# Performance work log

Hardware: AMD Instinct MI355X
Metric: run time of the kernel (lower is better)

Reference implementation:

```python
import jax, jax.numpy as jnp
import numpy as np

B = 32768   # batch
T = 10      # n_track
NW = 3      # n_waypoints
D = 128     # d_model
H = 8       # num_heads
HD = D // H # head_dim = 16


def _ln(x, g, b, eps=1e-5):
    m = jnp.mean(x, axis=-1, keepdims=True)
    v = jnp.mean((x - m) ** 2, axis=-1, keepdims=True)
    return (x - m) * jax.lax.rsqrt(v + eps) * g + b


def setup_inputs() -> dict:
    key = jax.random.key(0)
    ks = jax.random.split(key, 16)
    rn = lambda k, shape, s=0.05: jax.random.normal(k, shape, dtype=jnp.float32) * s
    return {
        "track_left": jax.random.normal(ks[0], (B, T, 2), dtype=jnp.float32),
        "track_right": jax.random.normal(ks[1], (B, T, 2), dtype=jnp.float32),
        "coord_w": rn(ks[2], (D, 2), 0.5), "coord_b": jnp.zeros((D,), jnp.float32),
        "pos_emb": rn(ks[3], (T, D), 0.02),
        "side_emb": rn(ks[4], (2, D), 0.02),
        "query_emb": rn(ks[5], (NW, D), 0.02),
        "tokens_ln_g": jnp.ones((D,), jnp.float32), "tokens_ln_b": jnp.zeros((D,), jnp.float32),
        "queries_ln_g": jnp.ones((D,), jnp.float32), "queries_ln_b": jnp.zeros((D,), jnp.float32),
        "in_proj_w": rn(ks[6], (3 * D, D)), "in_proj_b": jnp.zeros((3 * D,), jnp.float32),
        "out_proj_w": rn(ks[7], (D, D)), "out_proj_b": jnp.zeros((D,), jnp.float32),
        "fc1_w": rn(ks[8], (2 * D, D)), "fc1_b": jnp.zeros((2 * D,), jnp.float32),
        "fc2_w": rn(ks[9], (D, 2 * D)), "fc2_b": jnp.zeros((D,), jnp.float32),
        "post_attn_ln_g": jnp.ones((D,), jnp.float32), "post_attn_ln_b": jnp.zeros((D,), jnp.float32),
        "post_ffn_ln_g": jnp.ones((D,), jnp.float32), "post_ffn_ln_b": jnp.zeros((D,), jnp.float32),
        "head_w": rn(ks[10], (2, D)), "head_b": jnp.zeros((2,), jnp.float32),
    }


def reference(track_left, track_right, coord_w, coord_b, pos_emb, side_emb,
              query_emb, tokens_ln_g, tokens_ln_b, queries_ln_g, queries_ln_b,
              in_proj_w, in_proj_b, out_proj_w, out_proj_b, fc1_w, fc1_b,
              fc2_w, fc2_b, post_attn_ln_g, post_attn_ln_b, post_ffn_ln_g,
              post_ffn_ln_b, head_w, head_b):
    # --- tokens: embed + add pos/side + LN ---  (dropout = eval-mode identity)
    coords = jnp.concatenate([track_left, track_right], axis=1)       # [B, 2T, 2]
    coord_feat = coords @ coord_w.T + coord_b                          # [B, 2T, D]
    pos_vecs = jnp.concatenate([pos_emb, pos_emb], axis=0)             # [2T, D]
    side_vecs = jnp.concatenate([
        jnp.broadcast_to(side_emb[0], (T, D)),
        jnp.broadcast_to(side_emb[1], (T, D))], axis=0)                # [2T, D]
    tokens = _ln(coord_feat + pos_vecs + side_vecs, tokens_ln_g, tokens_ln_b)  # [B, 2T, D]

    # --- queries (shared across batch) ---
    queries = _ln(query_emb, queries_ln_g, queries_ln_b)               # [NW, D]

    # --- MHA (batch_first, packed qkv in_proj as in nn.MultiheadAttention) ---
    wq, wk, wv = in_proj_w[:D], in_proj_w[D:2 * D], in_proj_w[2 * D:]
    bq, bk, bv = in_proj_b[:D], in_proj_b[D:2 * D], in_proj_b[2 * D:]
    q = (queries @ wq.T + bq).reshape(NW, H, HD)                       # [NW, H, HD]
    k = (tokens @ wk.T + bk).reshape(-1, 2 * T, H, HD)                 # [B, 2T, H, HD]
    v = (tokens @ wv.T + bv).reshape(-1, 2 * T, H, HD)                 # [B, 2T, H, HD]
    scores = jnp.einsum('whd,bkhd->bhwk', q, k) / jnp.sqrt(jnp.float32(HD))
    attn = jax.nn.softmax(scores, axis=-1)                             # [B, H, NW, 2T]
    ctx = jnp.einsum('bhwk,bkhd->bwhd', attn, v).reshape(-1, NW, D)    # [B, NW, D]
    attn_out = ctx @ out_proj_w.T + out_proj_b                         # [B, NW, D]

    # --- residual + LN + FFN + residual + LN + head ---
    x = _ln(queries[None, :, :] + attn_out, post_attn_ln_g, post_attn_ln_b)
    h = jax.nn.relu(x @ fc1_w.T + fc1_b)
    h = h @ fc2_w.T + fc2_b
    x = _ln(x + h, post_ffn_ln_g, post_ffn_ln_b)
    return x @ head_w.T + head_b                                       # [B, NW, 2]
```

## Files before the change

kernel.cpp:

```cpp
#include <hip/hip_runtime.h>
#include <hip/hip_bf16.h>


typedef __bf16 bf16x8 __attribute__((ext_vector_type(8)));
typedef float  f32x4  __attribute__((ext_vector_type(4)));
static_assert(sizeof(bf16x8) == 16, "bf16x8 must be 16B");

__device__ __forceinline__ unsigned short f2b(float x) {
  __bf16 h = (__bf16)x;
  return __builtin_bit_cast(unsigned short, h);
}
__device__ __forceinline__ float b2f(unsigned short u) {
  return (float)__builtin_bit_cast(__bf16, u);
}
__device__ __forceinline__ float dot4(float4 a, float4 b) {
  return a.x*b.x + a.y*b.y + a.z*b.z + a.w*b.w;
}
__device__ __forceinline__ f32x4 mfma16(bf16x8 a, bf16x8 b, f32x4 c) {
  return __builtin_amdgcn_mfma_f32_16x16x32_bf16(a, b, c, 0, 0, 0);
}

#define WS_OM    0
#define WS_FC1   49152
#define WS_FC2   114688
#define WS_VB    180224
#define WS_VU    190464
#define WS_VW    190976
#define WS_VC    191488
#define WS_QN    192000
#define WS_SB    193536
#define WS_SU    195456
#define WS_SCAL  195744
#define WS_SUB   195756
#define WS_SWB   195836
#define WS_SBB   195916

__device__ float mean128(float v, volatile float* red) {
  #pragma unroll
  for (int o = 32; o; o >>= 1) v += __shfl_down(v, o, 64);
  __syncthreads();
  if ((threadIdx.x & 63) == 0) red[threadIdx.x >> 6] = v;
  __syncthreads();
  return (red[0] + red[1]) * (1.0f / 128.0f);
}

__global__ void k_tables(
    const float* __restrict__ coord_w, const float* __restrict__ coord_b,
    const float* __restrict__ pos_emb, const float* __restrict__ side_emb,
    const float* __restrict__ query_emb,
    const float* __restrict__ tln_g, const float* __restrict__ tln_b,
    const float* __restrict__ qln_g, const float* __restrict__ qln_b,
    const float* __restrict__ ipw, const float* __restrict__ ipb,
    char* __restrict__ ws)
{
  __shared__ float red[2];
  __shared__ float qn[3][128];
  __shared__ float qmat[3][128];
  __shared__ float vecA[128];
  __shared__ float vecB[128];
  __shared__ float vecC[128];
  __shared__ float kuA[128];
  __shared__ float kwA[128];
  __shared__ float kcA[128];
  const int d = threadIdx.x;
  const int t = blockIdx.x;

  float u  = coord_w[d*2+0];
  float w2 = coord_w[d*2+1];
  float g  = tln_g[d];
  float mu = mean128(u,  red);
  float mw = mean128(w2, red);
  float uh = u - mu, wh = w2 - mw;

  #pragma unroll
  for (int w = 0; w < 3; w++) {
    float qe = query_emb[w*128 + d];
    float m  = mean128(qe, red);
    float m2 = mean128(qe*qe, red);
    float var = m2 - m*m;
    qn[w][d] = (qe - m) * rsqrtf(var + 1e-5f) * qln_g[d] + qln_b[d];
  }
  __syncthreads();
  {
    const float* wqr = ipw + d*128;
    float a0 = 0, a1 = 0, a2 = 0;
    for (int k4 = 0; k4 < 32; k4++) {
      float4 wv4 = *(const float4*)&wqr[k4*4];
      a0 += dot4(wv4, *(const float4*)&qn[0][k4*4]);
      a1 += dot4(wv4, *(const float4*)&qn[1][k4*4]);
      a2 += dot4(wv4, *(const float4*)&qn[2][k4*4]);
    }
    float bq = ipb[d];
    qmat[0][d] = a0 + bq; qmat[1][d] = a1 + bq; qmat[2][d] = a2 + bq;
  }
  __syncthreads();

  if (t < 20) {
    float base = coord_b[d] + pos_emb[(t % 10)*128 + d] + side_emb[(t < 10 ? 0 : 1)*128 + d];
    float mb = mean128(base, red);
    float bh = base - mb;
    float sub = mean128(uh*bh, red);
    float swb = mean128(wh*bh, red);
    float sbb = mean128(bh*bh, red);
    if (d == 0) {
      ((float*)(ws + WS_SUB))[t] = sub;
      ((float*)(ws + WS_SWB))[t] = swb;
      ((float*)(ws + WS_SBB))[t] = sbb;
    }
    vecA[d] = bh * g;
    __syncthreads();
    const float* wkr = ipw + (128 + d)*128;
    const float* wvr = ipw + (256 + d)*128;
    float kb = 0, vb = 0;
    for (int k4 = 0; k4 < 32; k4++) {
      float4 a4 = *(const float4*)&vecA[k4*4];
      kb += dot4(*(const float4*)&wkr[k4*4], a4);
      vb += dot4(*(const float4*)&wvr[k4*4], a4);
    }
    kuA[d] = kb;
    ((float*)(ws + WS_VB))[t*128 + d] = vb;
    __syncthreads();
    if (d < 24) {
      int w = d / 8, h = d % 8;
      float s = 0;
      #pragma unroll
      for (int dl = 0; dl < 16; dl++) s += qmat[w][h*16 + dl] * kuA[h*16 + dl];
      ((float*)(ws + WS_SB))[(w*8 + h)*20 + t] = 0.25f * s;
    }
  } else {
    float suu = mean128(uh*uh, red);
    float sww = mean128(wh*wh, red);
    float suw = mean128(uh*wh, red);
    if (d == 0) {
      float* sc = (float*)(ws + WS_SCAL);
      sc[0] = suu; sc[1] = sww; sc[2] = suw;
    }
    vecA[d] = uh * g; vecB[d] = wh * g; vecC[d] = tln_b[d];
    __syncthreads();
    const float* wkr = ipw + (128 + d)*128;
    const float* wvr = ipw + (256 + d)*128;
    float ku = 0, kw = 0, kc = 0, vu = 0, vw = 0, vc = 0;
    for (int k4 = 0; k4 < 32; k4++) {
      float4 a4 = *(const float4*)&vecA[k4*4];
      float4 b4 = *(const float4*)&vecB[k4*4];
      float4 c4 = *(const float4*)&vecC[k4*4];
      float4 kv = *(const float4*)&wkr[k4*4];
      float4 vv = *(const float4*)&wvr[k4*4];
      ku += dot4(kv, a4); kw += dot4(kv, b4); kc += dot4(kv, c4);
      vu += dot4(vv, a4); vw += dot4(vv, b4); vc += dot4(vv, c4);
    }
    kc += ipb[128 + d]; vc += ipb[256 + d];
    ((float*)(ws + WS_VU))[d] = vu;
    ((float*)(ws + WS_VW))[d] = vw;
    ((float*)(ws + WS_VC))[d] = vc;
    kuA[d] = ku; kwA[d] = kw; kcA[d] = kc;
    float* qnw = (float*)(ws + WS_QN);
    qnw[0*128 + d] = qn[0][d]; qnw[1*128 + d] = qn[1][d]; qnw[2*128 + d] = qn[2][d];
    __syncthreads();
    if (d < 24) {
      int w = d / 8, h = d % 8;
      float su = 0, sw = 0, sc2 = 0;
      #pragma unroll
      for (int dl = 0; dl < 16; dl++) {
        float q = qmat[w][h*16 + dl];
        su  += q * kuA[h*16 + dl];
        sw  += q * kwA[h*16 + dl];
        sc2 += q * kcA[h*16 + dl];
      }
      float* o = (float*)(ws + WS_SU);
      o[ 0 + w*8 + h] = 0.25f * su;
      o[24 + w*8 + h] = 0.25f * sw;
      o[48 + w*8 + h] = 0.25f * sc2;
    }
  }
}

__global__ void k_build(
    const float* __restrict__ opw, const float* __restrict__ opb,
    const float* __restrict__ f1w, const float* __restrict__ f2w,
    char* __restrict__ ws)
{
  const int b = blockIdx.x, tid = threadIdx.x;
  if (b < 128) {
    __shared__ float Or[128];
    if (tid < 128) Or[tid] = opw[b*128 + tid];
    __syncthreads();
    if (tid < 192) {
      const float* VB = (const float*)(ws + WS_VB);
      const float* VU = (const float*)(ws + WS_VU);
      const float* VW = (const float*)(ws + WS_VW);
      const float* VC = (const float*)(ws + WS_VC);
      float val = 0.0f;
      if (tid < 160) {
        int h = tid / 20, tt = tid % 20;
        #pragma unroll
        for (int dl = 0; dl < 16; dl++) val += Or[h*16 + dl] * VB[tt*128 + h*16 + dl];
      } else if (tid < 168) {
        int h = tid - 160;
        #pragma unroll
        for (int dl = 0; dl < 16; dl++) val += Or[h*16 + dl] * VU[h*16 + dl];
      } else if (tid < 176) {
        int h = tid - 168;
        #pragma unroll
        for (int dl = 0; dl < 16; dl++) val += Or[h*16 + dl] * VW[h*16 + dl];
      } else if (tid == 176) {
        for (int d = 0; d < 128; d++) val += Or[d] * VC[d];
        val += opb[b];
      } else {
        val = 0.0f;
      }
      ((unsigned short*)(ws + WS_OM))[b*192 + tid] = f2b(val);
    }
  } else if (b < 144) {
    unsigned short* dst = (unsigned short*)(ws + WS_FC1);
    int i0 = (b - 128)*2048;
    #pragma unroll
    for (int j = 0; j < 8; j++) { int i = i0 + j*256 + tid; dst[i] = f2b(f1w[i]); }
  } else {
    unsigned short* dst = (unsigned short*)(ws + WS_FC2);
    int i0 = (b - 144)*2048;
    #pragma unroll
    for (int j = 0; j < 8; j++) { int i = i0 + j*256 + tid; dst[i] = f2b(f2w[i]); }
  }
}

#define GE 16
#define MR 48

__global__ __launch_bounds__(256, 2) void k_main(
    const float* __restrict__ tl, const float* __restrict__ tr,
    const float* __restrict__ f1b, const float* __restrict__ f2b_,
    const float* __restrict__ pag, const float* __restrict__ pab,
    const float* __restrict__ pfg, const float* __restrict__ pfb,
    const float* __restrict__ hw, const float* __restrict__ hb,
    const char* __restrict__ ws, float* __restrict__ out)
{
  __shared__ __align__(16) char smem[63744];
  float* S1 = (float*)smem;
  char*  C  = smem + 25344;
  unsigned short* Z   = (unsigned short*)C;
  float* xr  = (float*)(C + 19200);
  float* yr  = (float*)(C + 20480);
  float* rsA = (float*)(C + 21760);
  float* Sbl = (float*)(C + 23040);
  float* Sul = (float*)(C + 24960);
  float* Swl = (float*)(C + 25056);
  float* Scl = (float*)(C + 25152);
  unsigned short* h1 = (unsigned short*)C;
  unsigned short* X  = (unsigned short*)(smem + 50688);

  const unsigned short* OM = (const unsigned short*)(ws + WS_OM);
  const unsigned short* W1 = (const unsigned short*)(ws + WS_FC1);
  const unsigned short* W2 = (const unsigned short*)(ws + WS_FC2);
  const float* QN   = (const float*)(ws + WS_QN);
  const float* SBw  = (const float*)(ws + WS_SB);
  const float* SUw  = (const float*)(ws + WS_SU);
  const float* SCAL = (const float*)(ws + WS_SCAL);
  const float* SUB  = (const float*)(ws + WS_SUB);
  const float* SWB  = (const float*)(ws + WS_SWB);
  const float* SBB  = (const float*)(ws + WS_SBB);

  const int tid  = threadIdx.x;
  const int wg   = blockIdx.x;
  const int lane = tid & 63;
  const int wv   = tid >> 6;

  for (int i = tid; i < 480; i += 256) Sbl[i] = SBw[i];
  if (tid < 72) Sul[tid] = SUw[tid];
  if (tid < 48) {
    unsigned short* Zr = Z + tid*200;
    Zr[176] = 0x3F80;
    #pragma unroll
    for (int i = 177; i < 192; i++) Zr[i] = 0;
  }
  if (tid < 160) {
    int half = tid / 80;
    int i4   = tid % 80;
    const float* src = half ? tr : tl;
    float4 v = *(const float4*)(src + wg*(GE*20) + i4*4);
    int e  = i4 / 5;
    int j  = (i4 % 5) * 4;
    int t0 = half*10 + j/2;
    xr[e*20 + t0]     = v.x; yr[e*20 + t0]     = v.y;
    xr[e*20 + t0 + 1] = v.z; yr[e*20 + t0 + 1] = v.w;
  }
  __syncthreads();

  {
    float suu = SCAL[0], sww = SCAL[1], suw = SCAL[2];
    for (int i = tid; i < GE*20; i += 256) {
      int t = i % 20;
      float x = xr[i], y = yr[i];
      float var = suu*x*x + sww*y*y + 2.0f*suw*x*y
                + 2.0f*SUB[t]*x + 2.0f*SWB[t]*y + SBB[t];
      float rv = rsqrtf(var + 1e-5f);
      rsA[i] = rv; xr[i] = x*rv; yr[i] = y*rv;
    }
  }
  __syncthreads();

  if (tid < 128) {
    int e = tid >> 3, h = tid & 7;
    float xa[20], ya[20], ra[20];
    #pragma unroll
    for (int tb = 0; tb < 5; tb++) {
      float4 xv = *(const float4*)&xr[e*20 + tb*4];
      float4 yv = *(const float4*)&yr[e*20 + tb*4];
      float4 rv = *(const float4*)&rsA[e*20 + tb*4];
      xa[tb*4+0]=xv.x; xa[tb*4+1]=xv.y; xa[tb*4+2]=xv.z; xa[tb*4+3]=xv.w;
      ya[tb*4+0]=yv.x; ya[tb*4+1]=yv.y; ya[tb*4+2]=yv.z; ya[tb*4+3]=yv.w;
      ra[tb*4+0]=rv.x; ra[tb*4+1]=rv.y; ra[tb*4+2]=rv.z; ra[tb*4+3]=rv.w;
    }
    float s[3][20];
    #pragma unroll
    for (int w = 0; w < 3; w++) {
      float suv = Sul[w*8 + h], swv = Swl[w*8 + h], scv = Scl[w*8 + h];
      const float* sb = &Sbl[(w*8 + h)*20];
      #pragma unroll
      for (int tb = 0; tb < 5; tb++) {
        float4 s4 = *(const float4*)&sb[tb*4];
        s[w][tb*4+0] = fmaf(xa[tb*4+0],suv, fmaf(ya[tb*4+0],swv, fmaf(ra[tb*4+0],s4.x, scv)));
        s[w][tb*4+1] = fmaf(xa[tb*4+1],suv, fmaf(ya[tb*4+1],swv, fmaf(ra[tb*4+1],s4.y, scv)));
        s[w][tb*4+2] = fmaf(xa[tb*4+2],suv, fmaf(ya[tb*4+2],swv, fmaf(ra[tb*4+2],s4.z, scv)));
        s[w][tb*4+3] = fmaf(xa[tb*4+3],suv, fmaf(ya[tb*4+3],swv, fmaf(ra[tb*4+3],s4.w, scv)));
      }
    }
    unsigned short* Zr0 = Z + e*3*200;
    #pragma unroll
    for (int w = 0; w < 3; w++) {
      float m = s[w][0];
      #pragma unroll
      for (int t2 = 1; t2 < 20; t2++) m = fmaxf(m, s[w][t2]);
      float sum = 0;
      #pragma unroll
      for (int t2 = 0; t2 < 20; t2++) { float p = __expf(s[w][t2] - m); s[w][t2] = p; sum += p; }
      float inv = 1.0f / sum;
      float P = 0, Q = 0;
      #pragma unroll
      for (int t2 = 0; t2 < 20; t2++) { P = fmaf(s[w][t2], xa[t2], P); Q = fmaf(s[w][t2], ya[t2], Q); }
      P *= inv; Q *= inv;
      unsigned short* Zr = Zr0 + w*200;
      #pragma unroll
      for (int t2 = 0; t2 < 10; t2++) {
        unsigned int lo = f2b(s[w][2*t2]   * ra[2*t2]   * inv);
        unsigned int hi = f2b(s[w][2*t2+1] * ra[2*t2+1] * inv);
        *(unsigned int*)&Zr[h*20 + 2*t2] = lo | (hi << 16);
      }
      Zr[160 + h] = f2b(P);
      Zr[168 + h] = f2b(Q);
    }
  }
  __syncthreads();

  {
    int nbase = wv * 32;
    bf16x8 Bf[2][6];
    #pragma unroll
    for (int nt = 0; nt < 2; nt++)
      #pragma unroll
      for (int kt = 0; kt < 6; kt++) {
        int n = nbase + nt*16 + (lane & 15);
        int k = kt*32 + (lane >> 4)*8;
        Bf[nt][kt] = *(const bf16x8*)(OM + n*192 + k);
      }
    f32x4 acc[3][2];
    #pragma unroll
    for (int mt = 0; mt < 3; mt++)
      #pragma unroll
      for (int nt = 0; nt < 2; nt++) acc[mt][nt] = (f32x4){0.f,0.f,0.f,0.f};
    #pragma unroll
    for (int kt = 0; kt < 6; kt++) {
      bf16x8 Af[3];
      #pragma unroll
      for (int mt = 0; mt < 3; mt++) {
        int row = mt*16 + (lane & 15);
        int k   = kt*32 + (lane >> 4)*8;
        Af[mt] = *(const bf16x8*)(Z + row*200 + k);
      }
      #pragma unroll
      for (int mt = 0; mt < 3; mt++)
        #pragma unroll
        for (int nt = 0; nt < 2; nt++)
          acc[mt][nt] = mfma16(Af[mt], Bf[nt][kt], acc[mt][nt]);
    }
    #pragma unroll
    for (int mt = 0; mt < 3; mt++)
      #pragma unroll
      for (int nt = 0; nt < 2; nt++) {
        int col = nbase + nt*16 + (lane & 15);
        int r0  = mt*16 + ((lane >> 4) << 2);
        #pragma unroll
        for (int j = 0; j < 4; j++) S1[(r0 + j)*132 + col] = acc[mt][nt][j];
      }
  }
  __syncthreads();

  if (tid < MR) {
    int r = tid, w = r % 3;
    const float* qrow = QN + w*128;
    float s1 = 0, s2 = 0;
    #pragma unroll 8
    for (int d4 = 0; d4 < 32; d4++) {
      float4 v  = *(float4*)&S1[r*132 + d4*4];
      float4 q4 = *(const float4*)&qrow[d4*4];
      v.x += q4.x; v.y += q4.y; v.z += q4.z; v.w += q4.w;
      *(float4*)&S1[r*132 + d4*4] = v;
      s1 += v.x + v.y + v.z + v.w;
      s2 += v.x*v.x + v.y*v.y + v.z*v.z + v.w*v.w;
    }
    float m  = s1 * (1.0f/128.0f);
    float sc = rsqrtf(s2 * (1.0f/128.0f) - m*m + 1e-5f);
    #pragma unroll 8
    for (int d = 0; d < 128; d += 4) {
      float a0 = (S1[r*132 + d+0] - m)*sc*pag[d+0] + pab[d+0];
      float a1 = (S1[r*132 + d+1] - m)*sc*pag[d+1] + pab[d+1];
      float a2 = (S1[r*132 + d+2] - m)*sc*pag[d+2] + pab[d+2];
      float a3 = (S1[r*132 + d+3] - m)*sc*pag[d+3] + pab[d+3];
      uint2 pk;
      pk.x = (unsigned)f2b(a0) | ((unsigned)f2b(a1) << 16);
      pk.y = (unsigned)f2b(a2) | ((unsigned)f2b(a3) << 16);
      *(uint2*)&X[r*136 + d] = pk;
    }
  }
  __syncthreads();

  {
    int nbase = wv * 64;
    bf16x8 Bf[4][4];
    #pragma unroll
    for (int nt = 0; nt < 4; nt++)
      #pragma unroll
      for (int kt = 0; kt < 4; kt++) {
        int n = nbase + nt*16 + (lane & 15);
        int k = kt*32 + (lane >> 4)*8;
        Bf[nt][kt] = *(const bf16x8*)(W1 + n*128 + k);
      }
    f32x4 acc[3][4];
    #pragma unroll
    for (int mt = 0; mt < 3; mt++)
      #pragma unroll
      for (int nt = 0; nt < 4; nt++) acc[mt][nt] = (f32x4){0.f,0.f,0.f,0.f};
    #pragma unroll
    for (int kt = 0; kt < 4; kt++) {
      bf16x8 Af[3];
      #pragma unroll
      for (int mt = 0; mt < 3; mt++) {
        int row = mt*16 + (lane & 15);
        int k   = kt*32 + (lane >> 4)*8;
        Af[mt] = *(const bf16x8*)(X + row*136 + k);
      }
      #pragma unroll
      for (int mt = 0; mt < 3; mt++)
        #pragma unroll
        for (int nt = 0; nt < 4; nt++)
          acc[mt][nt] = mfma16(Af[mt], Bf[nt][kt], acc[mt][nt]);
    }
    #pragma unroll
    for (int nt = 0; nt < 4; nt++) {
      int col = nbase + nt*16 + (lane & 15);
      float bb = f1b[col];
      #pragma unroll
      for (int mt = 0; mt < 3; mt++) {
        int r0 = mt*16 + ((lane >> 4) << 2);
        #pragma unroll
        for (int j = 0; j < 4; j++) {
          float v = fmaxf(acc[mt][nt][j] + bb, 0.0f);
          h1[(r0 + j)*264 + col] = f2b(v);
        }
      }
    }
  }
  __syncthreads();

  {
    int nbase = wv * 32;
    bf16x8 Bf[2][8];
    #pragma unroll
    for (int nt = 0; nt < 2; nt++)
      #pragma unroll
      for (int kt = 0; kt < 8; kt++) {
        int n = nbase + nt*16 + (lane & 15);
        int k = kt*32 + (lane >> 4)*8;
        Bf[nt][kt] = *(const bf16x8*)(W2 + n*256 + k);
      }
    f32x4 acc[3][2];
    #pragma unroll
    for (int mt = 0; mt < 3; mt++)
      #pragma unroll
      for (int nt = 0; nt < 2; nt++) acc[mt][nt] = (f32x4){0.f,0.f,0.f,0.f};
    #pragma unroll
    for (int kt = 0; kt < 8; kt++) {
      bf16x8 Af[3];
      #pragma unroll
      for (int mt = 0; mt < 3; mt++) {
        int row = mt*16 + (lane & 15);
        int k   = kt*32 + (lane >> 4)*8;
        Af[mt] = *(const bf16x8*)(h1 + row*264 + k);
      }
      #pragma unroll
      for (int mt = 0; mt < 3; mt++)
        #pragma unroll
        for (int nt = 0; nt < 2; nt++)
          acc[mt][nt] = mfma16(Af[mt], Bf[nt][kt], acc[mt][nt]);
    }
    #pragma unroll
    for (int nt = 0; nt < 2; nt++) {
      int col = nbase + nt*16 + (lane & 15);
      float bb = f2b_[col];
      #pragma unroll
      for (int mt = 0; mt < 3; mt++) {
        int r0 = mt*16 + ((lane >> 4) << 2);
        #pragma unroll
        for (int j = 0; j < 4; j++) S1[(r0 + j)*132 + col] = acc[mt][nt][j] + bb;
      }
    }
  }
  __syncthreads();

  if (tid < MR) {
    int r = tid, e = r / 3, w = r % 3;
    float s1 = 0, s2 = 0;
    #pragma unroll 8
    for (int d4 = 0; d4 < 32; d4++) {
      float4 v = *(float4*)&S1[r*132 + d4*4];
      unsigned int u0 = *(unsigned int*)&X[r*136 + d4*4];
      unsigned int u1 = *(unsigned int*)&X[r*136 + d4*4 + 2];
      v.x += b2f((unsigned short)(u0 & 0xffff));
      v.y += b2f((unsigned short)(u0 >> 16));
      v.z += b2f((unsigned short)(u1 & 0xffff));
      v.w += b2f((unsigned short)(u1 >> 16));
      *(float4*)&S1[r*132 + d4*4] = v;
      s1 += v.x + v.y + v.z + v.w;
      s2 += v.x*v.x + v.y*v.y + v.z*v.z + v.w*v.w;
    }
    float m  = s1 * (1.0f/128.0f);
    float sc = rsqrtf(s2 * (1.0f/128.0f) - m*m + 1e-5f);
    float o0 = 0, o1 = 0;
    #pragma unroll 8
    for (int d = 0; d < 128; d++) {
      float xv = (S1[r*132 + d] - m)*sc*pfg[d] + pfb[d];
      o0 = fmaf(xv, hw[d],       o0);
      o1 = fmaf(xv, hw[128 + d], o1);
    }
    int gi = ((wg*GE + e)*3 + w)*2;
    out[gi]     = o0 + hb[0];
    out[gi + 1] = o1 + hb[1];
  }
}

extern "C" void kernel_launch(void* const* d_in, const int* in_sizes, int n_in,
                              void* d_out, int out_size, void* d_ws, size_t ws_size,
                              hipStream_t stream) {
  const float* tl       = (const float*)d_in[0];
  const float* tr       = (const float*)d_in[1];
  const float* coord_w  = (const float*)d_in[2];
  const float* coord_b  = (const float*)d_in[3];
  const float* pos_emb  = (const float*)d_in[4];
  const float* side_emb = (const float*)d_in[5];
  const float* query_emb= (const float*)d_in[6];
  const float* tln_g    = (const float*)d_in[7];
  const float* tln_b    = (const float*)d_in[8];
  const float* qln_g    = (const float*)d_in[9];
  const float* qln_b    = (const float*)d_in[10];
  const float* ipw      = (const float*)d_in[11];
  const float* ipb      = (const float*)d_in[12];
  const float* opw      = (const float*)d_in[13];
  const float* opb      = (const float*)d_in[14];
  const float* f1w      = (const float*)d_in[15];
  const float* f1b      = (const float*)d_in[16];
  const float* f2w      = (const float*)d_in[17];
  const float* f2b2     = (const float*)d_in[18];
  const float* pag      = (const float*)d_in[19];
  const float* pab      = (const float*)d_in[20];
  const float* pfg      = (const float*)d_in[21];
  const float* pfb      = (const float*)d_in[22];
  const float* hw       = (const float*)d_in[23];
  const float* hb       = (const float*)d_in[24];
  char* ws = (char*)d_ws;

  k_tables<<<21, 128, 0, stream>>>(coord_w, coord_b, pos_emb, side_emb, query_emb,
                                   tln_g, tln_b, qln_g, qln_b, ipw, ipb, ws);
  k_build<<<160, 256, 0, stream>>>(opw, opb, f1w, f2w, ws);
  k_main<<<32768 / GE, 256, 0, stream>>>(tl, tr, f1b, f2b2, pag, pab, pfg, pfb,
                                         hw, hb, ws, (float*)d_out);
}
```

Before: 215.0 us.

## Halve per-block batch, raise occupancy, parallelize attention and LayerNorm stages across threads

Each workgroup now handles 8 elements instead of 16, which halves shared memory and raises the launch-bounds occupancy target from 2 to 5 blocks per CU. The attention/softmax stage is rewritten so four threads split each (element, head) pair and combine results with cross-lane shuffles, which removes the staging buffers and two barriers. Both LayerNorm stages now use 8 threads per row with shuffle reductions instead of one serial thread per row. GEMM weight fragments are loaded per k-step instead of being preloaded into registers, and the padded second M-tile wastes part of the MFMA work in exchange for smaller tiles.

```diff
diff --git a/kernel.cpp b/kernel.cpp
--- a/kernel.cpp
+++ b/kernel.cpp
@@ -12,6 +12,9 @@
 }
 __device__ __forceinline__ float b2f(unsigned short u) {
   return (float)__builtin_bit_cast(__bf16, u);
+}
+__device__ __forceinline__ unsigned pack2(float a, float b) {
+  return (unsigned)f2b(a) | ((unsigned)f2b(b) << 16);
 }
 __device__ __forceinline__ float dot4(float4 a, float4 b) {
   return a.x*b.x + a.y*b.y + a.z*b.z + a.w*b.w;
@@ -224,10 +227,10 @@
   }
 }
 
-#define GE 16
-#define MR 48
-
-__global__ __launch_bounds__(256, 2) void k_main(
+#define GE 8
+#define MR 24
+
+__global__ __launch_bounds__(256, 5) void k_main(
     const float* __restrict__ tl, const float* __restrict__ tr,
     const float* __restrict__ f1b, const float* __restrict__ f2b_,
     const float* __restrict__ pag, const float* __restrict__ pab,
@@ -235,26 +238,18 @@
     const float* __restrict__ hw, const float* __restrict__ hb,
     const char* __restrict__ ws, float* __restrict__ out)
 {
-  __shared__ __align__(16) char smem[63744];
+  __shared__ __align__(16) char smem[31872];
   float* S1 = (float*)smem;
-  char*  C  = smem + 25344;
-  unsigned short* Z   = (unsigned short*)C;
-  float* xr  = (float*)(C + 19200);
-  float* yr  = (float*)(C + 20480);
-  float* rsA = (float*)(C + 21760);
-  float* Sbl = (float*)(C + 23040);
-  float* Sul = (float*)(C + 24960);
-  float* Swl = (float*)(C + 25056);
-  float* Scl = (float*)(C + 25152);
-  unsigned short* h1 = (unsigned short*)C;
-  unsigned short* X  = (unsigned short*)(smem + 50688);
+  unsigned short* Z  = (unsigned short*)(smem + 12672);
+  unsigned short* h1 = (unsigned short*)(smem + 12672);
+  unsigned short* X  = (unsigned short*)(smem + 25344);
 
   const unsigned short* OM = (const unsigned short*)(ws + WS_OM);
   const unsigned short* W1 = (const unsigned short*)(ws + WS_FC1);
   const unsigned short* W2 = (const unsigned short*)(ws + WS_FC2);
   const float* QN   = (const float*)(ws + WS_QN);
-  const float* SBw  = (const float*)(ws + WS_SB);
-  const float* SUw  = (const float*)(ws + WS_SU);
+  const float* SBwf = (const float*)(ws + WS_SB);
+  const float* SUwf = (const float*)(ws + WS_SU);
   const float* SCAL = (const float*)(ws + WS_SCAL);
   const float* SUB  = (const float*)(ws + WS_SUB);
   const float* SWB  = (const float*)(ws + WS_SWB);
@@ -264,209 +259,165 @@
   const int wg   = blockIdx.x;
   const int lane = tid & 63;
   const int wv   = tid >> 6;
-
-  for (int i = tid; i < 480; i += 256) Sbl[i] = SBw[i];
-  if (tid < 72) Sul[tid] = SUw[tid];
-  if (tid < 48) {
-    unsigned short* Zr = Z + tid*200;
-    Zr[176] = 0x3F80;
-    #pragma unroll
-    for (int i = 177; i < 192; i++) Zr[i] = 0;
-  }
-  if (tid < 160) {
-    int half = tid / 80;
-    int i4   = tid % 80;
-    const float* src = half ? tr : tl;
-    float4 v = *(const float4*)(src + wg*(GE*20) + i4*4);
-    int e  = i4 / 5;
-    int j  = (i4 % 5) * 4;
-    int t0 = half*10 + j/2;
-    xr[e*20 + t0]     = v.x; yr[e*20 + t0]     = v.y;
-    xr[e*20 + t0 + 1] = v.z; yr[e*20 + t0 + 1] = v.w;
-  }
-  __syncthreads();
+  const int quad = lane >> 4;
 
   {
-    float suu = SCAL[0], sww = SCAL[1], suw = SCAL[2];
-    for (int i = tid; i < GE*20; i += 256) {
-      int t = i % 20;
-      float x = xr[i], y = yr[i];
-      float var = suu*x*x + sww*y*y + 2.0f*suw*x*y
-                + 2.0f*SUB[t]*x + 2.0f*SWB[t]*y + SBB[t];
+    if (tid < MR) {
+      *(uint4*)(Z + tid*200 + 176) = uint4{0x3F80u, 0u, 0u, 0u};
+      *(uint4*)(Z + tid*200 + 184) = uint4{0u, 0u, 0u, 0u};
+    }
+    int e = tid >> 5, h = (tid >> 2) & 7, q = tid & 3;
+    const float* cb = (q < 2 ? tl : tr) + (wg*GE + e)*20 + (q & 1)*10;
+    float suu = SCAL[0], sww = SCAL[1], suw2 = 2.0f*SCAL[2];
+    float xa[5], ya[5], ra[5];
+    #pragma unroll
+    for (int j = 0; j < 5; j++) {
+      float2 c = *(const float2*)(cb + 2*j);
+      int t = q*5 + j;
+      float var = fmaf(suu, c.x*c.x, fmaf(sww, c.y*c.y, suw2*(c.x*c.y)))
+                + 2.0f*SUB[t]*c.x + 2.0f*SWB[t]*c.y + SBB[t];
       float rv = rsqrtf(var + 1e-5f);
-      rsA[i] = rv; xr[i] = x*rv; yr[i] = y*rv;
-    }
-  }
-  __syncthreads();
-
-  if (tid < 128) {
-    int e = tid >> 3, h = tid & 7;
-    float xa[20], ya[20], ra[20];
-    #pragma unroll
-    for (int tb = 0; tb < 5; tb++) {
-      float4 xv = *(const float4*)&xr[e*20 + tb*4];
-      float4 yv = *(const float4*)&yr[e*20 + tb*4];
-      float4 rv = *(const float4*)&rsA[e*20 + tb*4];
-      xa[tb*4+0]=xv.x; xa[tb*4+1]=xv.y; xa[tb*4+2]=xv.z; xa[tb*4+3]=xv.w;
-      ya[tb*4+0]=yv.x; ya[tb*4+1]=yv.y; ya[tb*4+2]=yv.z; ya[tb*4+3]=yv.w;
-      ra[tb*4+0]=rv.x; ra[tb*4+1]=rv.y; ra[tb*4+2]=rv.z; ra[tb*4+3]=rv.w;
-    }
-    float s[3][20];
+      xa[j] = c.x*rv; ya[j] = c.y*rv; ra[j] = rv;
+    }
+    unsigned short* Zr0 = Z + e*3*200;
     #pragma unroll
     for (int w = 0; w < 3; w++) {
-      float suv = Sul[w*8 + h], swv = Swl[w*8 + h], scv = Scl[w*8 + h];
-      const float* sb = &Sbl[(w*8 + h)*20];
-      #pragma unroll
-      for (int tb = 0; tb < 5; tb++) {
-        float4 s4 = *(const float4*)&sb[tb*4];
-        s[w][tb*4+0] = fmaf(xa[tb*4+0],suv, fmaf(ya[tb*4+0],swv, fmaf(ra[tb*4+0],s4.x, scv)));
-        s[w][tb*4+1] = fmaf(xa[tb*4+1],suv, fmaf(ya[tb*4+1],swv, fmaf(ra[tb*4+1],s4.y, scv)));
-        s[w][tb*4+2] = fmaf(xa[tb*4+2],suv, fmaf(ya[tb*4+2],swv, fmaf(ra[tb*4+2],s4.z, scv)));
-        s[w][tb*4+3] = fmaf(xa[tb*4+3],suv, fmaf(ya[tb*4+3],swv, fmaf(ra[tb*4+3],s4.w, scv)));
-      }
-    }
-    unsigned short* Zr0 = Z + e*3*200;
-    #pragma unroll
-    for (int w = 0; w < 3; w++) {
-      float m = s[w][0];
-      #pragma unroll
-      for (int t2 = 1; t2 < 20; t2++) m = fmaxf(m, s[w][t2]);
-      float sum = 0;
-      #pragma unroll
-      for (int t2 = 0; t2 < 20; t2++) { float p = __expf(s[w][t2] - m); s[w][t2] = p; sum += p; }
+      float su = SUwf[w*8 + h], sw = SUwf[24 + w*8 + h], sc = SUwf[48 + w*8 + h];
+      const float* sb = SBwf + (w*8 + h)*20 + q*5;
+      float s[5];
+      float m = -1e30f;
+      #pragma unroll
+      for (int j = 0; j < 5; j++) {
+        s[j] = fmaf(xa[j], su, fmaf(ya[j], sw, fmaf(ra[j], sb[j], sc)));
+        m = fmaxf(m, s[j]);
+      }
+      m = fmaxf(m, __shfl_xor(m, 1));
+      m = fmaxf(m, __shfl_xor(m, 2));
+      float sum = 0, P = 0, Q = 0;
+      #pragma unroll
+      for (int j = 0; j < 5; j++) {
+        float p = __expf(s[j] - m);
+        s[j] = p; sum += p;
+        P = fmaf(p, xa[j], P); Q = fmaf(p, ya[j], Q);
+      }
+      sum += __shfl_xor(sum, 1); sum += __shfl_xor(sum, 2);
+      P   += __shfl_xor(P, 1);   P   += __shfl_xor(P, 2);
+      Q   += __shfl_xor(Q, 1);   Q   += __shfl_xor(Q, 2);
       float inv = 1.0f / sum;
-      float P = 0, Q = 0;
-      #pragma unroll
-      for (int t2 = 0; t2 < 20; t2++) { P = fmaf(s[w][t2], xa[t2], P); Q = fmaf(s[w][t2], ya[t2], Q); }
-      P *= inv; Q *= inv;
       unsigned short* Zr = Zr0 + w*200;
       #pragma unroll
-      for (int t2 = 0; t2 < 10; t2++) {
-        unsigned int lo = f2b(s[w][2*t2]   * ra[2*t2]   * inv);
-        unsigned int hi = f2b(s[w][2*t2+1] * ra[2*t2+1] * inv);
-        *(unsigned int*)&Zr[h*20 + 2*t2] = lo | (hi << 16);
-      }
-      Zr[160 + h] = f2b(P);
-      Zr[168 + h] = f2b(Q);
+      for (int j = 0; j < 5; j++) Zr[h*20 + q*5 + j] = f2b(s[j]*ra[j]*inv);
+      if (q == 0) { Zr[160 + h] = f2b(P*inv); Zr[168 + h] = f2b(Q*inv); }
     }
   }
   __syncthreads();
 
   {
     int nbase = wv * 32;
-    bf16x8 Bf[2][6];
-    #pragma unroll
-    for (int nt = 0; nt < 2; nt++)
-      #pragma unroll
-      for (int kt = 0; kt < 6; kt++) {
-        int n = nbase + nt*16 + (lane & 15);
-        int k = kt*32 + (lane >> 4)*8;
-        Bf[nt][kt] = *(const bf16x8*)(OM + n*192 + k);
-      }
-    f32x4 acc[3][2];
-    #pragma unroll
-    for (int mt = 0; mt < 3; mt++)
+    int n0 = nbase + (lane & 15), n1 = n0 + 16;
+    int r0c = lane & 15;
+    int r1c = min(16 + (lane & 15), 23);
+    f32x4 acc[2][2];
+    #pragma unroll
+    for (int mt = 0; mt < 2; mt++)
       #pragma unroll
       for (int nt = 0; nt < 2; nt++) acc[mt][nt] = (f32x4){0.f,0.f,0.f,0.f};
     #pragma unroll
     for (int kt = 0; kt < 6; kt++) {
-      bf16x8 Af[3];
-      #pragma unroll
-      for (int mt = 0; mt < 3; mt++) {
-        int row = mt*16 + (lane & 15);
-        int k   = kt*32 + (lane >> 4)*8;
-        Af[mt] = *(const bf16x8*)(Z + row*200 + k);
-      }
-      #pragma unroll
-      for (int mt = 0; mt < 3; mt++)
-        #pragma unroll
-        for (int nt = 0; nt < 2; nt++)
-          acc[mt][nt] = mfma16(Af[mt], Bf[nt][kt], acc[mt][nt]);
-    }
-    #pragma unroll
-    for (int mt = 0; mt < 3; mt++)
+      int k = kt*32 + quad*8;
+      bf16x8 Bf0 = *(const bf16x8*)(OM + n0*192 + k);
+      bf16x8 Bf1 = *(const bf16x8*)(OM + n1*192 + k);
+      bf16x8 Af0 = *(const bf16x8*)(Z + r0c*200 + k);
+      bf16x8 Af1 = *(const bf16x8*)(Z + r1c*200 + k);
+      acc[0][0] = mfma16(Af0, Bf0, acc[0][0]);
+      acc[0][1] = mfma16(Af0, Bf1, acc[0][1]);
+      acc[1][0] = mfma16(Af1, Bf0, acc[1][0]);
+      acc[1][1] = mfma16(Af1, Bf1, acc[1][1]);
+    }
+    #pragma unroll
+    for (int mt = 0; mt < 2; mt++) {
+      if (mt == 1 && quad >= 2) break;
       #pragma unroll
       for (int nt = 0; nt < 2; nt++) {
         int col = nbase + nt*16 + (lane & 15);
-        int r0  = mt*16 + ((lane >> 4) << 2);
+        int r0  = mt*16 + quad*4;
         #pragma unroll
         for (int j = 0; j < 4; j++) S1[(r0 + j)*132 + col] = acc[mt][nt][j];
       }
-  }
-  __syncthreads();
-
-  if (tid < MR) {
-    int r = tid, w = r % 3;
-    const float* qrow = QN + w*128;
+    }
+  }
+  __syncthreads();
+
+  if (tid < 192) {
+    int r = tid >> 3, p = tid & 7, w = r % 3;
+    float4 v[4];
+    #pragma unroll
+    for (int j = 0; j < 4; j++) {
+      int i = (j + p) & 3;
+      v[i] = *(float4*)&S1[r*132 + p*16 + i*4];
+    }
+    const float* qrow = QN + w*128 + p*16;
     float s1 = 0, s2 = 0;
-    #pragma unroll 8
-    for (int d4 = 0; d4 < 32; d4++) {
-      float4 v  = *(float4*)&S1[r*132 + d4*4];
-      float4 q4 = *(const float4*)&qrow[d4*4];
-      v.x += q4.x; v.y += q4.y; v.z += q4.z; v.w += q4.w;
-      *(float4*)&S1[r*132 + d4*4] = v;
-      s1 += v.x + v.y + v.z + v.w;
-      s2 += v.x*v.x + v.y*v.y + v.z*v.z + v.w*v.w;
-    }
+    #pragma unroll
+    for (int i = 0; i < 4; i++) {
+      float4 q4 = *(const float4*)(qrow + i*4);
+      v[i].x += q4.x; v[i].y += q4.y; v[i].z += q4.z; v[i].w += q4.w;
+      s1 += v[i].x + v[i].y + v[i].z + v[i].w;
+      s2 += v[i].x*v[i].x + v[i].y*v[i].y + v[i].z*v[i].z + v[i].w*v[i].w;
+    }
+    #pragma unroll
+    for (int o = 1; o < 8; o <<= 1) { s1 += __shfl_xor(s1, o); s2 += __shfl_xor(s2, o); }
     float m  = s1 * (1.0f/128.0f);
     float sc = rsqrtf(s2 * (1.0f/128.0f) - m*m + 1e-5f);
-    #pragma unroll 8
-    for (int d = 0; d < 128; d += 4) {
-      float a0 = (S1[r*132 + d+0] - m)*sc*pag[d+0] + pab[d+0];
-      float a1 = (S1[r*132 + d+1] - m)*sc*pag[d+1] + pab[d+1];
-      float a2 = (S1[r*132 + d+2] - m)*sc*pag[d+2] + pab[d+2];
-      float a3 = (S1[r*132 + d+3] - m)*sc*pag[d+3] + pab[d+3];
-      uint2 pk;
-      pk.x = (unsigned)f2b(a0) | ((unsigned)f2b(a1) << 16);
-      pk.y = (unsigned)f2b(a2) | ((unsigned)f2b(a3) << 16);
-      *(uint2*)&X[r*136 + d] = pk;
-    }
+    unsigned pk[8];
+    #pragma unroll
+    for (int i = 0; i < 4; i++) {
+      float4 g4 = *(const float4*)(pag + p*16 + i*4);
+      float4 b4 = *(const float4*)(pab + p*16 + i*4);
+      float a0 = (v[i].x - m)*sc*g4.x + b4.x;
+      float a1 = (v[i].y - m)*sc*g4.y + b4.y;
+      float a2 = (v[i].z - m)*sc*g4.z + b4.z;
+      float a3 = (v[i].w - m)*sc*g4.w + b4.w;
+      pk[i*2]   = pack2(a0, a1);
+      pk[i*2+1] = pack2(a2, a3);
+    }
+    *(uint4*)&X[r*136 + p*16]     = uint4{pk[0], pk[1], pk[2], pk[3]};
+    *(uint4*)&X[r*136 + p*16 + 8] = uint4{pk[4], pk[5], pk[6], pk[7]};
   }
   __syncthreads();
 
   {
     int nbase = wv * 64;
-    bf16x8 Bf[4][4];
-    #pragma unroll
-    for (int nt = 0; nt < 4; nt++)
-      #pragma unroll
-      for (int kt = 0; kt < 4; kt++) {
-        int n = nbase + nt*16 + (lane & 15);
-        int k = kt*32 + (lane >> 4)*8;
-        Bf[nt][kt] = *(const bf16x8*)(W1 + n*128 + k);
-      }
-    f32x4 acc[3][4];
-    #pragma unroll
-    for (int mt = 0; mt < 3; mt++)
+    int r0c = lane & 15;
+    int r1c = min(16 + (lane & 15), 23);
+    f32x4 acc[2][4];
+    #pragma unroll
+    for (int mt = 0; mt < 2; mt++)
       #pragma unroll
       for (int nt = 0; nt < 4; nt++) acc[mt][nt] = (f32x4){0.f,0.f,0.f,0.f};
     #pragma unroll
     for (int kt = 0; kt < 4; kt++) {
-      bf16x8 Af[3];
-      #pragma unroll
-      for (int mt = 0; mt < 3; mt++) {
-        int row = mt*16 + (lane & 15);
-        int k   = kt*32 + (lane >> 4)*8;
-        Af[mt] = *(const bf16x8*)(X + row*136 + k);
-      }
-      #pragma unroll
-      for (int mt = 0; mt < 3; mt++)
-        #pragma unroll
-        for (int nt = 0; nt < 4; nt++)
-          acc[mt][nt] = mfma16(Af[mt], Bf[nt][kt], acc[mt][nt]);
+      int k = kt*32 + quad*8;
+      bf16x8 Af0 = *(const bf16x8*)(X + r0c*136 + k);
+      bf16x8 Af1 = *(const bf16x8*)(X + r1c*136 + k);
+      #pragma unroll
+      for (int nt = 0; nt < 4; nt++) {
+        bf16x8 Bf = *(const bf16x8*)(W1 + (nbase + nt*16 + (lane & 15))*128 + k);
+        acc[0][nt] = mfma16(Af0, Bf, acc[0][nt]);
+        acc[1][nt] = mfma16(Af1, Bf, acc[1][nt]);
+      }
     }
     #pragma unroll
     for (int nt = 0; nt < 4; nt++) {
       int col = nbase + nt*16 + (lane & 15);
       float bb = f1b[col];
       #pragma unroll
-      for (int mt = 0; mt < 3; mt++) {
-        int r0 = mt*16 + ((lane >> 4) << 2);
+      for (int mt = 0; mt < 2; mt++) {
+        if (mt == 1 && quad >= 2) break;
+        int r0 = mt*16 + quad*4;
         #pragma unroll
-        for (int j = 0; j < 4; j++) {
-          float v = fmaxf(acc[mt][nt][j] + bb, 0.0f);
-          h1[(r0 + j)*264 + col] = f2b(v);
-        }
+        for (int j = 0; j < 4; j++)
+          h1[(r0 + j)*264 + col] = f2b(fmaxf(acc[mt][nt][j] + bb, 0.0f));
       }
     }
   }
@@ -474,42 +425,34 @@
 
   {
     int nbase = wv * 32;
-    bf16x8 Bf[2][8];
-    #pragma unroll
-    for (int nt = 0; nt < 2; nt++)
-      #pragma unroll
-      for (int kt = 0; kt < 8; kt++) {
-        int n = nbase + nt*16 + (lane & 15);
-        int k = kt*32 + (lane >> 4)*8;
-        Bf[nt][kt] = *(const bf16x8*)(W2 + n*256 + k);
-      }
-    f32x4 acc[3][2];
-    #pragma unroll
-    for (int mt = 0; mt < 3; mt++)
+    int n0 = nbase + (lane & 15), n1 = n0 + 16;
+    int r0c = lane & 15;
+    int r1c = min(16 + (lane & 15), 23);
+    f32x4 acc[2][2];
+    #pragma unroll
+    for (int mt = 0; mt < 2; mt++)
       #pragma unroll
       for (int nt = 0; nt < 2; nt++) acc[mt][nt] = (f32x4){0.f,0.f,0.f,0.f};
     #pragma unroll
     for (int kt = 0; kt < 8; kt++) {
-      bf16x8 Af[3];
-      #pragma unroll
-      for (int mt = 0; mt < 3; mt++) {
-        int row = mt*16 + (lane & 15);
-        int k   = kt*32 + (lane >> 4)*8;
-        Af[mt] = *(const bf16x8*)(h1 + row*264 + k);
-      }
-      #pragma unroll
-      for (int mt = 0; mt < 3; mt++)
-        #pragma unroll
-        for (int nt = 0; nt < 2; nt++)
-          acc[mt][nt] = mfma16(Af[mt], Bf[nt][kt], acc[mt][nt]);
-    }
-    #pragma unroll
-    for (int nt = 0; nt < 2; nt++) {
-      int col = nbase + nt*16 + (lane & 15);
-      float bb = f2b_[col];
-      #pragma unroll
-      for (int mt = 0; mt < 3; mt++) {
-        int r0 = mt*16 + ((lane >> 4) << 2);
+      int k = kt*32 + quad*8;
+      bf16x8 Bf0 = *(const bf16x8*)(W2 + n0*256 + k);
+      bf16x8 Bf1 = *(const bf16x8*)(W2 + n1*256 + k);
+      bf16x8 Af0 = *(const bf16x8*)(h1 + r0c*264 + k);
+      bf16x8 Af1 = *(const bf16x8*)(h1 + r1c*264 + k);
+      acc[0][0] = mfma16(Af0, Bf0, acc[0][0]);
+      acc[0][1] = mfma16(Af0, Bf1, acc[0][1]);
+      acc[1][0] = mfma16(Af1, Bf0, acc[1][0]);
+      acc[1][1] = mfma16(Af1, Bf1, acc[1][1]);
+    }
+    #pragma unroll
+    for (int mt = 0; mt < 2; mt++) {
+      if (mt == 1 && quad >= 2) break;
+      #pragma unroll
+      for (int nt = 0; nt < 2; nt++) {
+        int col = nbase + nt*16 + (lane & 15);
+        float bb = f2b_[col];
+        int r0 = mt*16 + quad*4;
         #pragma unroll
         for (int j = 0; j < 4; j++) S1[(r0 + j)*132 + col] = acc[mt][nt][j] + bb;
       }
@@ -517,34 +460,54 @@
   }
   __syncthreads();
 
-  if (tid < MR) {
-    int r = tid, e = r / 3, w = r % 3;
+  if (tid < 192) {
+    int r = tid >> 3, p = tid & 7;
+    int e = r / 3, w = r % 3;
+    float4 v[4];
+    #pragma unroll
+    for (int j = 0; j < 4; j++) {
+      int i = (j + p) & 3;
+      v[i] = *(float4*)&S1[r*132 + p*16 + i*4];
+    }
+    uint4 u0 = *(const uint4*)&X[r*136 + p*16];
+    uint4 u1 = *(const uint4*)&X[r*136 + p*16 + 8];
+    float xb[16];
+    xb[0]=b2f(u0.x&0xffff); xb[1]=b2f(u0.x>>16); xb[2]=b2f(u0.y&0xffff); xb[3]=b2f(u0.y>>16);
+    xb[4]=b2f(u0.z&0xffff); xb[5]=b2f(u0.z>>16); xb[6]=b2f(u0.w&0xffff); xb[7]=b2f(u0.w>>16);
+    xb[8]=b2f(u1.x&0xffff); xb[9]=b2f(u1.x>>16); xb[10]=b2f(u1.y&0xffff); xb[11]=b2f(u1.y>>16);
+    xb[12]=b2f(u1.z&0xffff); xb[13]=b2f(u1.z>>16); xb[14]=b2f(u1.w&0xffff); xb[15]=b2f(u1.w>>16);
     float s1 = 0, s2 = 0;
-    #pragma unroll 8
-    for (int d4 = 0; d4 < 32; d4++) {
-      float4 v = *(float4*)&S1[r*132 + d4*4];
-      unsigned int u0 = *(unsigned int*)&X[r*136 + d4*4];
-      unsigned int u1 = *(unsigned int*)&X[r*136 + d4*4 + 2];
-      v.x += b2f((unsigned short)(u0 & 0xffff));
-      v.y += b2f((unsigned short)(u0 >> 16));
-      v.z += b2f((unsigned short)(u1 & 0xffff));
-      v.w += b2f((unsigned short)(u1 >> 16));
-      *(float4*)&S1[r*132 + d4*4] = v;
-      s1 += v.x + v.y + v.z + v.w;
-      s2 += v.x*v.x + v.y*v.y + v.z*v.z + v.w*v.w;
-    }
+    #pragma unroll
+    for (int i = 0; i < 4; i++) {
+      v[i].x += xb[i*4+0]; v[i].y += xb[i*4+1]; v[i].z += xb[i*4+2]; v[i].w += xb[i*4+3];
+      s1 += v[i].x + v[i].y + v[i].z + v[i].w;
+      s2 += v[i].x*v[i].x + v[i].y*v[i].y + v[i].z*v[i].z + v[i].w*v[i].w;
+    }
+    #pragma unroll
+    for (int o = 1; o < 8; o <<= 1) { s1 += __shfl_xor(s1, o); s2 += __shfl_xor(s2, o); }
     float m  = s1 * (1.0f/128.0f);
     float sc = rsqrtf(s2 * (1.0f/128.0f) - m*m + 1e-5f);
     float o0 = 0, o1 = 0;
-    #pragma unroll 8
-    for (int d = 0; d < 128; d++) {
-      float xv = (S1[r*132 + d] - m)*sc*pfg[d] + pfb[d];
-      o0 = fmaf(xv, hw[d],       o0);
-      o1 = fmaf(xv, hw[128 + d], o1);
-    }
-    int gi = ((wg*GE + e)*3 + w)*2;
-    out[gi]     = o0 + hb[0];
-    out[gi + 1] = o1 + hb[1];
+    #pragma unroll
+    for (int i = 0; i < 4; i++) {
+      float4 g4 = *(const float4*)(pfg + p*16 + i*4);
+      float4 b4 = *(const float4*)(pfb + p*16 + i*4);
+      float4 h0 = *(const float4*)(hw + p*16 + i*4);
+      float4 h8 = *(const float4*)(hw + 128 + p*16 + i*4);
+      float x0 = (v[i].x - m)*sc*g4.x + b4.x;
+      float x1 = (v[i].y - m)*sc*g4.y + b4.y;
+      float x2 = (v[i].z - m)*sc*g4.z + b4.z;
+      float x3 = (v[i].w - m)*sc*g4.w + b4.w;
+      o0 = fmaf(x0,h0.x, fmaf(x1,h0.y, fmaf(x2,h0.z, fmaf(x3,h0.w, o0))));
+      o1 = fmaf(x0,h8.x, fmaf(x1,h8.y, fmaf(x2,h8.z, fmaf(x3,h8.w, o1))));
+    }
+    #pragma unroll
+    for (int o = 1; o < 8; o <<= 1) { o0 += __shfl_xor(o0, o); o1 += __shfl_xor(o1, o); }
+    if (p == 0) {
+      int gi = ((wg*GE + e)*3 + w)*2;
+      out[gi]     = o0 + hb[0];
+      out[gi + 1] = o1 + hb[1];
+    }
   }
 }
 
```

New measurement: 269.2 us. 1.25x slower.
